# Optimization experiments

Hardware: AMD Instinct MI355X
Metric: run time of the kernel (lower is better)

The kernel has to match this reference:

```python
import jax, jax.numpy as jnp
import numpy as np

B, L, D_MODEL = 2, 2048, 1024
D_STATE, D_CONV, EXPAND = 8, 4, 2
D_INNER = EXPAND * D_MODEL          # 2048
DT_RANK = (D_MODEL + 15) // 16      # 64


def setup_inputs() -> dict:
    key = jax.random.key(0)
    ks = jax.random.split(key, 8)
    s = 0.02
    x = jax.random.normal(ks[0], (B, L, D_MODEL), dtype=jnp.float32)
    W_in = jax.random.normal(ks[1], (D_MODEL, 2 * D_INNER), dtype=jnp.float32) * s
    dw_kernel = jax.random.normal(ks[2], (D_CONV, D_INNER), dtype=jnp.float32) * s  # depthwise
    pw_kernel = jax.random.normal(ks[3], (D_INNER, D_INNER), dtype=jnp.float32) * s  # pointwise
    conv_bias = jnp.zeros((D_INNER,), dtype=jnp.float32)
    W_x = jax.random.normal(ks[4], (D_INNER, DT_RANK + 2 * D_STATE), dtype=jnp.float32) * s
    W_dt = jax.random.normal(ks[5], (DT_RANK, D_INNER), dtype=jnp.float32) * s
    b_dt = jnp.zeros((D_INNER,), dtype=jnp.float32)
    # A = repeat(range(1..d_state), d_inner).reshape(d_inner, d_state), stored as log
    A_init = np.repeat(np.arange(1, D_STATE + 1, dtype=np.float32), D_INNER).reshape(D_INNER, D_STATE)
    A_log = jnp.asarray(np.log(A_init))
    D = jnp.ones((D_INNER,), dtype=jnp.float32)
    W_out = jax.random.normal(ks[6], (D_INNER, D_MODEL), dtype=jnp.float32) * s
    return {"x": x, "W_in": W_in, "dw_kernel": dw_kernel, "pw_kernel": pw_kernel,
            "conv_bias": conv_bias, "W_x": W_x, "W_dt": W_dt, "b_dt": b_dt,
            "A_log": A_log, "D": D, "W_out": W_out}


def reference(x, W_in, dw_kernel, pw_kernel, conv_bias, W_x, W_dt, b_dt, A_log, D, W_out):
    d_inner, d_state = A_log.shape
    dt_rank = W_dt.shape[0]
    d_conv = dw_kernel.shape[0]
    bsz = x.shape[0]

    xz = x @ W_in                                   # [B,L,2*di]
    x_in, z = jnp.split(xz, 2, axis=-1)             # each [B,L,di]

    # causal separable conv: depthwise (causal pad) -> pointwise -> swish
    xp = jnp.pad(x_in, ((0, 0), (d_conv - 1, 0), (0, 0)))
    xc = jax.lax.conv_general_dilated(
        xp, dw_kernel[:, None, :], window_strides=(1,), padding='VALID',
        dimension_numbers=('NWC', 'WIO', 'NWC'), feature_group_count=d_inner)
    xc = jax.nn.silu(xc @ pw_kernel + conv_bias)    # [B,L,di]

    x_dbl = xc @ W_x                                # [B,L,dt_rank+2*ds]
    delta = x_dbl[..., :dt_rank]
    Bm = x_dbl[..., dt_rank:dt_rank + d_state]      # [B,L,ds]
    C = x_dbl[..., dt_rank + d_state:]              # [B,L,ds]
    delta = jax.nn.softplus(delta @ W_dt + b_dt)    # [B,L,di]

    A = -jnp.exp(A_log)                             # [di,ds]
    deltaA = jnp.exp(jnp.einsum('bld,dn->bldn', delta, A))       # [B,L,di,ds]
    deltaB_u = jnp.einsum('bld,bln,bld->bldn', delta, Bm, xc)    # [B,L,di,ds]

    def step(h, inp):
        dA_t, dBu_t, C_t = inp
        h = dA_t * h + dBu_t                        # [B,di,ds]
        y_t = jnp.einsum('bn,bdn->bd', C_t, h)      # [B,di]
        return h, y_t

    h0 = jnp.zeros((bsz, d_inner, d_state), dtype=x.dtype)
    elems = (deltaA.transpose(1, 0, 2, 3), deltaB_u.transpose(1, 0, 2, 3), C.transpose(1, 0, 2))
    _, ys = jax.lax.scan(step, h0, elems)           # ys: [L,B,di]
    y = ys.transpose(1, 0, 2)                       # [B,L,di]

    y = y + xc * D
    y = y * jax.nn.silu(z)
    return y @ W_out                                # [B,L,d_model]
```

## Files before the change

kernel.cpp:

```cpp
#include <hip/hip_runtime.h>
#include <math.h>

#define Bb 2
#define Ll 2048
#define DMODEL 1024
#define DINNER 2048
#define DSTATE 8
#define DTRANK 64
#define DCONV 4
#define MM (Bb*Ll)
#define NCH 64
#define CL 32
#define G3_KCH 8
#define G3_KC (DINNER / G3_KCH)

typedef __attribute__((ext_vector_type(8))) short    bf16x8;
typedef __attribute__((ext_vector_type(4))) float    f32x4;

__device__ __forceinline__ float silu_f(float x) {
    return x / (1.0f + __expf(-x));
}
__device__ __forceinline__ float softplus_f(float x) {
    return fmaxf(x, 0.0f) + log1pf(__expf(-fabsf(x)));
}
__device__ __forceinline__ unsigned short f2bf(float f) {
    unsigned int u = __float_as_uint(f);
    u += 0x7fffu + ((u >> 16) & 1u);
    return (unsigned short)(u >> 16);
}
__device__ __forceinline__ float bf2f(unsigned short u) {
    return __uint_as_float(((unsigned int)u) << 16);
}
__device__ __forceinline__ void async_cp16(const unsigned short* g, unsigned short* l) {
    __builtin_amdgcn_global_load_lds(
        (const __attribute__((address_space(1))) void*)g,
        (__attribute__((address_space(3))) void*)l, 16, 0, 0);
}

template <int EPI, int NW, int TN, typename OT, int RX = 0, int RY = 1>
__global__ __launch_bounds__(NW * 64, 4) void mfma_gemm(
    const unsigned short* __restrict__ A, const unsigned short* __restrict__ Bt,
    OT* __restrict__ C, OT* __restrict__ C2, int nsplit,
    int M, int N, int K, int lda, int ldb, int ldc,
    const float* __restrict__ bias)
{
    constexpr int NT   = NW * 64;
    constexpr int WNC  = NW / 2;
    constexpr int WNE  = TN / WNC;
    constexpr int NJ   = WNE / 16;
    constexpr int RPP  = NT / 4;
    constexpr int APASS = 128 / RPP;
    constexpr int BPASS = TN / RPP;

    __shared__ unsigned short As[2][128 * 32];
    __shared__ unsigned short Bs[2][TN * 32];

    int bxx = blockIdx.x, byy = blockIdx.y;
    if constexpr (RX > 0) {
        const int f = blockIdx.y * gridDim.x + blockIdx.x;
        const int c = f & 7, q = f >> 3;
        const int rgw = gridDim.x / RX;
        bxx = (c % rgw) * RX + (q % RX);
        byy = (c / rgw) * RY + (q / RX);
    }
    const int bm = byy * 128;
    const int bn = bxx * TN;
    const int tid  = threadIdx.x;
    const int w    = tid >> 6;
    const int lane = tid & 63;
    const int wm = (w / WNC) * 64;
    const int wn = (w % WNC) * WNE;
    const int lr = lane & 15;
    const int lq = lane >> 4;

    const int row  = tid >> 2;
    const int sp   = tid & 3;
    const int slog = sp ^ ((row >> 1) & 3);
    const unsigned short* gA = A  + (size_t)(bm + row) * lda + slog * 8;
    const unsigned short* gB = Bt + (size_t)(bn + row) * ldb + slog * 8;
    const int st = tid * 8;

    const int fsw = (lq ^ ((lr >> 1) & 3)) * 8;

    f32x4 acc[4][NJ];
#pragma unroll
    for (int i = 0; i < 4; ++i)
#pragma unroll
        for (int j = 0; j < NJ; ++j) acc[i][j] = (f32x4){0.f, 0.f, 0.f, 0.f};

#pragma unroll
    for (int p = 0; p < APASS; ++p)
        async_cp16(gA + (size_t)p * RPP * lda, &As[0][p * RPP * 32 + st]);
#pragma unroll
    for (int p = 0; p < BPASS; ++p)
        async_cp16(gB + (size_t)p * RPP * ldb, &Bs[0][p * RPP * 32 + st]);

    int cur = 0;
    for (int k0 = 0; k0 < K; k0 += 32, cur ^= 1) {
        __syncthreads();
        const int nk = k0 + 32;
        if (nk < K) {
            const int nb = cur ^ 1;
#pragma unroll
            for (int p = 0; p < APASS; ++p)
                async_cp16(gA + (size_t)p * RPP * lda + nk, &As[nb][p * RPP * 32 + st]);
#pragma unroll
            for (int p = 0; p < BPASS; ++p)
                async_cp16(gB + (size_t)p * RPP * ldb + nk, &Bs[nb][p * RPP * 32 + st]);
        }

        bf16x8 a[4], b[NJ];
#pragma unroll
        for (int i = 0; i < 4; ++i)
            a[i] = *(const bf16x8*)&As[cur][(wm + i * 16 + lr) * 32 + fsw];
#pragma unroll
        for (int j = 0; j < NJ; ++j)
            b[j] = *(const bf16x8*)&Bs[cur][(wn + j * 16 + lr) * 32 + fsw];
#pragma unroll
        for (int i = 0; i < 4; ++i)
#pragma unroll
            for (int j = 0; j < NJ; ++j)
                acc[i][j] = __builtin_amdgcn_mfma_f32_16x16x32_bf16(
                    a[i], b[j], acc[i][j], 0, 0, 0);
    }

#pragma unroll
    for (int i = 0; i < 4; ++i) {
        const int row0 = bm + wm + i * 16 + lq * 4;
#pragma unroll
        for (int j = 0; j < NJ; ++j) {
            const int col = bn + wn + j * 16 + lr;
            OT* Cb; int colb;
            if (col < nsplit) { Cb = C; colb = col; }
            else              { Cb = C2; colb = col - nsplit; }
            float bv = (EPI != 0) ? bias[col] : 0.0f;
#pragma unroll
            for (int r = 0; r < 4; ++r) {
                float v = acc[i][j][r];
                if (EPI == 1) v = silu_f(v + bv);
                if (EPI == 2) v = softplus_f(v + bv);
                if (sizeof(OT) == 2)
                    Cb[(size_t)(row0 + r) * ldc + colb] = (OT)f2bf(v);
                else
                    Cb[(size_t)(row0 + r) * ldc + colb] = (OT)v;
            }
        }
    }
}

template <bool I1, bool I2, int VMA, int VMB>
__device__ __forceinline__ void g1_tile(
    int kt, const unsigned short* __restrict__ gA,
    const unsigned short* __restrict__ gB, int lda, int ldb,
    unsigned short* As, unsigned short* Bs, int st,
    int wm, int wn, int lr, int fsw, f32x4 (&acc)[8][4])
{
    const int cur = kt & 1;
    const int sb0 = (cur << 1) * 8192;
    const int sb1 = ((cur << 1) | 1) * 8192;
    const int nb1 = ((kt + 1) & 1) << 1;
    const int nb2 = ((kt + 2) & 1) << 1;
    bf16x8 a[4], b[4];

#pragma unroll
    for (int i = 0; i < 4; ++i)
        a[i] = *(const bf16x8*)&As[sb0 + (wm + i * 16 + lr) * 32 + fsw];
#pragma unroll
    for (int j = 0; j < 4; ++j)
        b[j] = *(const bf16x8*)&Bs[sb0 + (wn + j * 16 + lr) * 32 + fsw];
    if (I1) {
        const unsigned short* s = gA + (kt + 1) * 64 + 32;
        unsigned short* d = &As[(nb1 | 1) * 8192 + st];
        async_cp16(s, d);
        async_cp16(s + (size_t)128 * lda, d + 4096);
        __builtin_amdgcn_sched_barrier(0);
    }
    __builtin_amdgcn_s_barrier();
    asm volatile("s_waitcnt lgkmcnt(0)" ::: "memory");
    __builtin_amdgcn_sched_barrier(0);
    __builtin_amdgcn_s_setprio(1);
#pragma unroll
    for (int i = 0; i < 4; ++i)
#pragma unroll
        for (int j = 0; j < 4; ++j)
            acc[i][j] = __builtin_amdgcn_mfma_f32_16x16x32_bf16(
                a[i], b[j], acc[i][j], 0, 0, 0);
    __builtin_amdgcn_s_setprio(0);
    __builtin_amdgcn_s_barrier();

#pragma unroll
    for (int i = 0; i < 4; ++i)
        a[i] = *(const bf16x8*)&As[sb0 + (wm + (4 + i) * 16 + lr) * 32 + fsw];
    if (I1) {
        const unsigned short* s = gB + (kt + 1) * 64 + 32;
        unsigned short* d = &Bs[(nb1 | 1) * 8192 + st];
        async_cp16(s, d);
        async_cp16(s + (size_t)128 * ldb, d + 4096);
        __builtin_amdgcn_sched_barrier(0);
    }
    __builtin_amdgcn_s_barrier();
    asm volatile("s_waitcnt lgkmcnt(0)" ::: "memory");
    __builtin_amdgcn_sched_barrier(0);
    __builtin_amdgcn_s_setprio(1);
#pragma unroll
    for (int i = 0; i < 4; ++i)
#pragma unroll
        for (int j = 0; j < 4; ++j)
            acc[4 + i][j] = __builtin_amdgcn_mfma_f32_16x16x32_bf16(
                a[i], b[j], acc[4 + i][j], 0, 0, 0);
    __builtin_amdgcn_s_setprio(0);
    asm volatile("s_waitcnt vmcnt(%0)" :: "n"(VMA) : "memory");
    __builtin_amdgcn_s_barrier();

#pragma unroll
    for (int i = 0; i < 4; ++i)
        a[i] = *(const bf16x8*)&As[sb1 + (wm + i * 16 + lr) * 32 + fsw];
#pragma unroll
    for (int j = 0; j < 4; ++j)
        b[j] = *(const bf16x8*)&Bs[sb1 + (wn + j * 16 + lr) * 32 + fsw];
    if (I2) {
        const unsigned short* s = gA + (kt + 2) * 64;
        unsigned short* d = &As[nb2 * 8192 + st];
        async_cp16(s, d);
        async_cp16(s + (size_t)128 * lda, d + 4096);
        __builtin_amdgcn_sched_barrier(0);
    }
    __builtin_amdgcn_s_barrier();
    asm volatile("s_waitcnt lgkmcnt(0)" ::: "memory");
    __builtin_amdgcn_sched_barrier(0);
    __builtin_amdgcn_s_setprio(1);
#pragma unroll
    for (int i = 0; i < 4; ++i)
#pragma unroll
        for (int j = 0; j < 4; ++j)
            acc[i][j] = __builtin_amdgcn_mfma_f32_16x16x32_bf16(
                a[i], b[j], acc[i][j], 0, 0, 0);
    __builtin_amdgcn_s_setprio(0);
    __builtin_amdgcn_s_barrier();

#pragma unroll
    for (int i = 0; i < 4; ++i)
        a[i] = *(const bf16x8*)&As[sb1 + (wm + (4 + i) * 16 + lr) * 32 + fsw];
    if (I2) {
        const unsigned short* s = gB + (kt + 2) * 64;
        unsigned short* d = &Bs[nb2 * 8192 + st];
        async_cp16(s, d);
        async_cp16(s + (size_t)128 * ldb, d + 4096);
        __builtin_amdgcn_sched_barrier(0);
    }
    __builtin_amdgcn_s_barrier();
    asm volatile("s_waitcnt lgkmcnt(0)" ::: "memory");
    __builtin_amdgcn_sched_barrier(0);
    __builtin_amdgcn_s_setprio(1);
#pragma unroll
    for (int i = 0; i < 4; ++i)
#pragma unroll
        for (int j = 0; j < 4; ++j)
            acc[4 + i][j] = __builtin_amdgcn_mfma_f32_16x16x32_bf16(
                a[i], b[j], acc[4 + i][j], 0, 0, 0);
    __builtin_amdgcn_s_setprio(0);
    asm volatile("s_waitcnt vmcnt(%0)" :: "n"(VMB) : "memory");
    __builtin_amdgcn_s_barrier();
}

__global__ __launch_bounds__(512, 2) void gemm256_g1(
    const unsigned short* __restrict__ A, const unsigned short* __restrict__ Bt,
    unsigned short* __restrict__ Cx, unsigned short* __restrict__ Cz,
    int K, int lda, int ldb, int ldc, int nsplit)
{
    __shared__ unsigned short As[4 * 8192];
    __shared__ unsigned short Bs[4 * 8192];

    int bx, by;
    {
        const int f = blockIdx.y * gridDim.x + blockIdx.x;
        const int c = f & 7, q = f >> 3;
        const int rgw = gridDim.x >> 3;
        bx = (c % rgw) * 8 + (q & 7);
        by = (c / rgw) * 4 + (q >> 3);
    }
    const int bm = by * 256, bn = bx * 256;
    const int tid  = threadIdx.x;
    const int lane = tid & 63;
    const int w    = tid >> 6;
    const int wm = (w >> 2) << 7;
    const int wn = (w & 3) << 6;
    const int lr = lane & 15;
    const int lq = lane >> 4;
    const int fsw = (lq ^ ((lr >> 1) & 3)) * 8;

    const int row  = tid >> 2;
    const int slog = (tid & 3) ^ ((row >> 1) & 3);
    const unsigned short* gA = A  + (size_t)(bm + row) * lda + slog * 8;
    const unsigned short* gB = Bt + (size_t)(bn + row) * ldb + slog * 8;
    const int st = tid * 8;
    const int NT = K >> 6;

    f32x4 acc[8][4];
#pragma unroll
    for (int i = 0; i < 8; ++i)
#pragma unroll
        for (int j = 0; j < 4; ++j) acc[i][j] = (f32x4){0.f, 0.f, 0.f, 0.f};

    auto stg = [&](const unsigned short* g, int ld, unsigned short* d) {
        async_cp16(g, d);
        async_cp16(g + (size_t)128 * ld, d + 4096);
    };
    stg(gA,      lda, As + 0 * 8192 + st);
    __builtin_amdgcn_sched_barrier(0);
    stg(gB,      ldb, Bs + 0 * 8192 + st);
    __builtin_amdgcn_sched_barrier(0);
    stg(gA + 32, lda, As + 1 * 8192 + st);
    __builtin_amdgcn_sched_barrier(0);
    stg(gB + 32, ldb, Bs + 1 * 8192 + st);
    __builtin_amdgcn_sched_barrier(0);
    stg(gA + 64, lda, As + 2 * 8192 + st);
    __builtin_amdgcn_sched_barrier(0);
    stg(gB + 64, ldb, Bs + 2 * 8192 + st);
    asm volatile("s_waitcnt vmcnt(8)" ::: "memory");
    __builtin_amdgcn_sched_barrier(0);
    __builtin_amdgcn_s_barrier();

    for (int kt = 0; kt + 2 < NT; ++kt)
        g1_tile<true, true, 8, 8>(kt, gA, gB, lda, ldb,
                                  As, Bs, st, wm, wn, lr, fsw, acc);
    g1_tile<true,  false, 8, 4>(NT - 2, gA, gB, lda, ldb,
                                As, Bs, st, wm, wn, lr, fsw, acc);
    g1_tile<false, false, 0, 0>(NT - 1, gA, gB, lda, ldb,
                                As, Bs, st, wm, wn, lr, fsw, acc);

#pragma unroll
    for (int i = 0; i < 8; ++i) {
        const int row0 = bm + wm + i * 16 + lq * 4;
#pragma unroll
        for (int j = 0; j < 4; ++j) {
            const int col = bn + wn + j * 16 + lr;
            unsigned short* Cb; int colb;
            if (col < nsplit) { Cb = Cx; colb = col; }
            else              { Cb = Cz; colb = col - nsplit; }
#pragma unroll
            for (int r = 0; r < 4; ++r)
                Cb[(size_t)(row0 + r) * ldc + colb] = f2bf(acc[i][j][r]);
        }
    }
}

template <bool I1, bool I2, int VMA, int VMB>
__device__ __forceinline__ void g2c_tile(
    int kt, const unsigned short* __restrict__ gA,
    const unsigned short* __restrict__ gB, int lda, int ldb,
    unsigned short* As, unsigned short* Bs, int st,
    int wm, int wn, int lr, int fsw, f32x4 (&acc)[4][4])
{
    const int cur = kt & 1;
    const int sa0 = (cur << 1) * 4096;
    const int sa1 = ((cur << 1) | 1) * 4096;
    const int sb0 = (cur << 1) * 4096;
    const int sb1 = ((cur << 1) | 1) * 4096;
    const int nb1 = (((kt + 1) & 1) << 1) | 1;
    const int nb2 = ((kt + 2) & 1) << 1;
    bf16x8 a[4], b[4];

#pragma unroll
    for (int i = 0; i < 4; ++i)
        a[i] = *(const bf16x8*)&As[sa0 + (wm + i * 16 + lr) * 32 + fsw];
#pragma unroll
    for (int j = 0; j < 4; ++j)
        b[j] = *(const bf16x8*)&Bs[sb0 + (wn + j * 16 + lr) * 32 + fsw];
    if (I1) {
        const unsigned short* sA = gA + (kt + 1) * 64 + 32;
        unsigned short* dA = &As[nb1 * 4096 + st];
        async_cp16(sA, dA);
        async_cp16(sA + (size_t)64 * lda, dA + 2048);
        const unsigned short* sB = gB + (kt + 1) * 64 + 32;
        unsigned short* dB = &Bs[nb1 * 4096 + st];
        async_cp16(sB, dB);
        async_cp16(sB + (size_t)64 * ldb, dB + 2048);
        __builtin_amdgcn_sched_barrier(0);
    }
    __builtin_amdgcn_s_barrier();
    asm volatile("s_waitcnt lgkmcnt(0)" ::: "memory");
    __builtin_amdgcn_sched_barrier(0);
    __builtin_amdgcn_s_setprio(1);
#pragma unroll
    for (int i = 0; i < 4; ++i)
#pragma unroll
        for (int j = 0; j < 4; ++j)
            acc[i][j] = __builtin_amdgcn_mfma_f32_16x16x32_bf16(
                a[i], b[j], acc[i][j], 0, 0, 0);
    __builtin_amdgcn_s_setprio(0);
    asm volatile("s_waitcnt vmcnt(%0)" :: "n"(VMA) : "memory");
    __builtin_amdgcn_s_barrier();

#pragma unroll
    for (int i = 0; i < 4; ++i)
        a[i] = *(const bf16x8*)&As[sa1 + (wm + i * 16 + lr) * 32 + fsw];
#pragma unroll
    for (int j = 0; j < 4; ++j)
        b[j] = *(const bf16x8*)&Bs[sb1 + (wn + j * 16 + lr) * 32 + fsw];
    if (I2) {
        const unsigned short* sA = gA + (kt + 2) * 64;
        unsigned short* dA = &As[nb2 * 4096 + st];
        async_cp16(sA, dA);
        async_cp16(sA + (size_t)64 * lda, dA + 2048);
        const unsigned short* sB = gB + (kt + 2) * 64;
        unsigned short* dB = &Bs[nb2 * 4096 + st];
        async_cp16(sB, dB);
        async_cp16(sB + (size_t)64 * ldb, dB + 2048);
        __builtin_amdgcn_sched_barrier(0);
    }
    __builtin_amdgcn_s_barrier();
    asm volatile("s_waitcnt lgkmcnt(0)" ::: "memory");
    __builtin_amdgcn_sched_barrier(0);
    __builtin_amdgcn_s_setprio(1);
#pragma unroll
    for (int i = 0; i < 4; ++i)
#pragma unroll
        for (int j = 0; j < 4; ++j)
            acc[i][j] = __builtin_amdgcn_mfma_f32_16x16x32_bf16(
                a[i], b[j], acc[i][j], 0, 0, 0);
    __builtin_amdgcn_s_setprio(0);
    asm volatile("s_waitcnt vmcnt(%0)" :: "n"(VMB) : "memory");
    __builtin_amdgcn_s_barrier();
}

template <int EPI, typename OT>
__global__ __launch_bounds__(256, 2) void gemm128x128(
    const unsigned short* __restrict__ A, const unsigned short* __restrict__ Bt,
    OT* __restrict__ C, int K, int lda, int ldb, int ldc,
    const float* __restrict__ bias)
{
    __shared__ unsigned short As[4 * 4096];
    __shared__ unsigned short Bs[4 * 4096];

    int bx, by;
    {
        const int f = blockIdx.y * gridDim.x + blockIdx.x;
        const int c = f & 7, q = f >> 3;
        const int rgw = gridDim.x >> 3;
        bx = (c % rgw) * 8 + (q & 7);
        by = (c / rgw) * 8 + (q >> 3);
    }
    const int bm = by * 128, bn = bx * 128;
    const int tid  = threadIdx.x;
    const int lane = tid & 63;
    const int w    = tid >> 6;
    const int wm = (w >> 1) << 6;
    const int wn = (w & 1) << 6;
    const int lr = lane & 15;
    const int lq = lane >> 4;
    const int fsw = (lq ^ ((lr >> 1) & 3)) * 8;

    const int row  = tid >> 2;
    const int slog = (tid & 3) ^ ((row >> 1) & 3);
    const unsigned short* gA = A  + (size_t)(bm + row) * lda + slog * 8;
    const unsigned short* gB = Bt + (size_t)(bn + row) * ldb + slog * 8;
    const int st = tid * 8;
    const int NT = K >> 6;

    f32x4 acc[4][4];
#pragma unroll
    for (int i = 0; i < 4; ++i)
#pragma unroll
        for (int j = 0; j < 4; ++j) acc[i][j] = (f32x4){0.f, 0.f, 0.f, 0.f};

    auto stg = [&](int ko, int slot) {
        const unsigned short* sA = gA + ko;
        unsigned short* dA = &As[slot * 4096 + st];
        async_cp16(sA, dA);
        async_cp16(sA + (size_t)64 * lda, dA + 2048);
        const unsigned short* sB = gB + ko;
        unsigned short* dB = &Bs[slot * 4096 + st];
        async_cp16(sB, dB);
        async_cp16(sB + (size_t)64 * ldb, dB + 2048);
    };
    stg(0, 0);
    __builtin_amdgcn_sched_barrier(0);
    stg(32, 1);
    __builtin_amdgcn_sched_barrier(0);
    stg(64, 2);
    asm volatile("s_waitcnt vmcnt(8)" ::: "memory");
    __builtin_amdgcn_sched_barrier(0);
    __builtin_amdgcn_s_barrier();

    for (int kt = 0; kt + 2 < NT; ++kt)
        g2c_tile<true, true, 8, 8>(kt, gA, gB, lda, ldb,
                                   As, Bs, st, wm, wn, lr, fsw, acc);
    g2c_tile<true,  false, 8, 4>(NT - 2, gA, gB, lda, ldb,
                                 As, Bs, st, wm, wn, lr, fsw, acc);
    g2c_tile<false, false, 0, 0>(NT - 1, gA, gB, lda, ldb,
                                 As, Bs, st, wm, wn, lr, fsw, acc);

#pragma unroll
    for (int i = 0; i < 4; ++i) {
        const int row0 = bm + wm + i * 16 + lq * 4;
#pragma unroll
        for (int j = 0; j < 4; ++j) {
            const int col = bn + wn + j * 16 + lr;
            float bv = (EPI != 0) ? bias[col] : 0.0f;
#pragma unroll
            for (int r = 0; r < 4; ++r) {
                float v = acc[i][j][r];
                if (EPI == 1) v = silu_f(v + bv);
                if (EPI == 2) v = softplus_f(v + bv);
                if (sizeof(OT) == 2)
                    C[(size_t)(row0 + r) * ldc + col] = (OT)f2bf(v);
                else
                    C[(size_t)(row0 + r) * ldc + col] = (OT)v;
            }
        }
    }
}

__global__ __launch_bounds__(256) void prep_all(
    const float* __restrict__ x, const float* __restrict__ W_in,
    const float* __restrict__ pwk, const float* __restrict__ W_out,
    const float* __restrict__ W_dt,
    unsigned short* __restrict__ x_bf, unsigned short* __restrict__ Wint,
    unsigned short* __restrict__ pw_t, unsigned short* __restrict__ Woutt,
    unsigned short* __restrict__ Wdtt)
{
    const int b = blockIdx.x;
    const int t = threadIdx.x;
    if (b < 4096) {
        int i = b * 1024 + t * 4;
        float4 v = *(const float4*)&x[i];
        ushort4 o;
        o.x = f2bf(v.x); o.y = f2bf(v.y); o.z = f2bf(v.z); o.w = f2bf(v.w);
        *(ushort4*)&x_bf[i] = o;
        return;
    }
    const float* src; unsigned short* dst; int R, C, c0, r0;
    if (b < 8192) {
        int bi = b - 4096; src = W_in; dst = Wint; R = 1024; C = 4096;
        c0 = (bi & 127) * 32; r0 = (bi >> 7) * 32;
    } else if (b < 12288) {
        int bi = b - 8192; src = pwk; dst = pw_t; R = 2048; C = 2048;
        c0 = (bi & 63) * 32; r0 = (bi >> 6) * 32;
    } else if (b < 14336) {
        int bi = b - 12288; src = W_out; dst = Woutt; R = 2048; C = 1024;
        c0 = (bi & 31) * 32; r0 = (bi >> 5) * 32;
    } else {
        int bi = b - 14336; src = W_dt; dst = Wdtt; R = 64; C = 2048;
        c0 = (bi & 63) * 32; r0 = (bi >> 6) * 32;
    }
    __shared__ float tile[32][33];
    const int tx = t & 31;
    const int ty = t >> 5;
#pragma unroll
    for (int i = 0; i < 32; i += 8)
        tile[ty + i][tx] = src[(size_t)(r0 + ty + i) * C + c0 + tx];
    __syncthreads();
#pragma unroll
    for (int i = 0; i < 32; i += 8)
        dst[(size_t)(c0 + ty + i) * R + r0 + tx] = f2bf(tile[tx][ty + i]);
}

__global__ __launch_bounds__(256) void g3_splitk(
    const unsigned short* __restrict__ xc, const float* __restrict__ Wx,
    float* __restrict__ part)
{
    __shared__ float As[16][68];
    __shared__ float Bs[16][85];
    const int m0 = blockIdx.x * 64;
    const int kb = blockIdx.y * G3_KC;
    const int t = threadIdx.x;
    const int tr = t >> 4;
    const int tc = t & 15;

    const int arow = t >> 2;
    const int ak4  = (t & 3) * 4;
    const int bk   = t >> 4;
    const int bc   = (t & 15) * 5;

    float acc[4][5];
#pragma unroll
    for (int r = 0; r < 4; ++r)
#pragma unroll
        for (int c = 0; c < 5; ++c) acc[r][c] = 0.0f;

    for (int k0 = 0; k0 < G3_KC; k0 += 16) {
        ushort4 av = *(const ushort4*)&xc[(size_t)(m0 + arow) * DINNER + kb + k0 + ak4];
        float bv[5];
#pragma unroll
        for (int q = 0; q < 5; ++q)
            bv[q] = Wx[(size_t)(kb + k0 + bk) * 80 + bc + q];
        __syncthreads();
        As[ak4 + 0][arow] = bf2f(av.x);
        As[ak4 + 1][arow] = bf2f(av.y);
        As[ak4 + 2][arow] = bf2f(av.z);
        As[ak4 + 3][arow] = bf2f(av.w);
#pragma unroll
        for (int q = 0; q < 5; ++q) Bs[bk][bc + q] = bv[q];
        __syncthreads();
#pragma unroll
        for (int k = 0; k < 16; ++k) {
            float a[4], b[5];
#pragma unroll
            for (int r = 0; r < 4; ++r) a[r] = As[k][tr * 4 + r];
#pragma unroll
            for (int c = 0; c < 5; ++c) b[c] = Bs[k][tc * 5 + c];
#pragma unroll
            for (int r = 0; r < 4; ++r)
#pragma unroll
                for (int c = 0; c < 5; ++c)
                    acc[r][c] = fmaf(a[r], b[c], acc[r][c]);
        }
    }
#pragma unroll
    for (int r = 0; r < 4; ++r)
#pragma unroll
        for (int c = 0; c < 5; ++c)
            part[((size_t)blockIdx.y * MM + m0 + tr * 4 + r) * 80 + tc * 5 + c] = acc[r][c];
}

__global__ __launch_bounds__(256) void g3_reduce(
    const float* __restrict__ part, float* __restrict__ xdbl,
    unsigned short* __restrict__ xdbl64)
{
    int i = (blockIdx.x * 256 + threadIdx.x) * 4;
    if (i >= MM * 80) return;
    float4 s = *(const float4*)&part[i];
#pragma unroll
    for (int c = 1; c < G3_KCH; ++c) {
        float4 p = *(const float4*)&part[(size_t)c * MM * 80 + i];
        s.x += p.x; s.y += p.y; s.z += p.z; s.w += p.w;
    }
    *(float4*)&xdbl[i] = s;
    int col = i % 80;
    if (col < 64) {
        int row = i / 80;
        ushort4 o;
        o.x = f2bf(s.x); o.y = f2bf(s.y); o.z = f2bf(s.z); o.w = f2bf(s.w);
        *(ushort4*)&xdbl64[(size_t)row * 64 + col] = o;
    }
}

__global__ __launch_bounds__(256) void dwconv_kernel(
    const unsigned short* __restrict__ x_in, const float* __restrict__ dwk,
    unsigned short* __restrict__ out)
{
    int i4 = blockIdx.x * 256 + threadIdx.x;
    if (i4 >= MM * DINNER / 4) return;
    int d = (i4 * 4) & (DINNER - 1);
    int bl = (i4 * 4) >> 11;
    int l = bl & (Ll - 1);
    int b = bl >> 11;
    float a0 = 0.f, a1 = 0.f, a2 = 0.f, a3 = 0.f;
#pragma unroll
    for (int k = 0; k < DCONV; ++k) {
        int t = l + k - (DCONV - 1);
        if (t >= 0) {
            ushort4 xv = *(const ushort4*)&x_in[(size_t)(b * Ll + t) * DINNER + d];
            float4 wv = *(const float4*)&dwk[k * DINNER + d];
            a0 = fmaf(bf2f(xv.x), wv.x, a0);
            a1 = fmaf(bf2f(xv.y), wv.y, a1);
            a2 = fmaf(bf2f(xv.z), wv.z, a2);
            a3 = fmaf(bf2f(xv.w), wv.w, a3);
        }
    }
    ushort4 o;
    o.x = f2bf(a0); o.y = f2bf(a1); o.z = f2bf(a2); o.w = f2bf(a3);
    *(ushort4*)&out[i4 * 4] = o;
}

__global__ __launch_bounds__(256) void scan_pass1(
    const float* __restrict__ delta, const unsigned short* __restrict__ xc,
    const float* __restrict__ xdbl, const float* __restrict__ A_log,
    float* __restrict__ cs_a, float* __restrict__ cs_h)
{
    const int d = blockIdx.x * 256 + threadIdx.x;
    const int c = blockIdx.y;
    const int b = blockIdx.z;
    const int t0 = c * CL;

    __shared__ float sB[CL][8];
    {
        int i = threadIdx.x;
        int t = i >> 3, j = i & 7;
        sB[t][j] = xdbl[((size_t)(b * Ll + t0 + t)) * 80 + DTRANK + j];
    }
    __syncthreads();

    float An[8];
#pragma unroll
    for (int n = 0; n < 8; ++n) An[n] = -__expf(A_log[d * 8 + n]);

    float h[8], ap[8];
#pragma unroll
    for (int n = 0; n < 8; ++n) { h[n] = 0.0f; ap[n] = 1.0f; }

    const float* dptr = delta + ((size_t)(b * Ll + t0)) * DINNER + d;
    const unsigned short* xptr = xc + ((size_t)(b * Ll + t0)) * DINNER + d;

#pragma unroll 4
    for (int t = 0; t < CL; ++t) {
        float dl = dptr[(size_t)t * DINNER];
        float xv = bf2f(xptr[(size_t)t * DINNER]);
        float du = dl * xv;
#pragma unroll
        for (int n = 0; n < 8; ++n) {
            float dA = __expf(dl * An[n]);
            h[n] = fmaf(dA, h[n], du * sB[t][n]);
            ap[n] *= dA;
        }
    }

    size_t base = (((size_t)(b * NCH + c)) * 8) * DINNER + d;
#pragma unroll
    for (int n = 0; n < 8; ++n) {
        cs_a[base + (size_t)n * DINNER] = ap[n];
        cs_h[base + (size_t)n * DINNER] = h[n];
    }
}

__global__ __launch_bounds__(256) void scan_pass2(
    const float* __restrict__ cs_a, const float* cs_h, float* hin)
{
    int idx = blockIdx.x * 256 + threadIdx.x;
    if (idx >= Bb * 8 * DINNER) return;
    int d = idx & (DINNER - 1);
    int n = (idx >> 11) & 7;
    int b = idx >> 14;
    float H = 0.0f;
#pragma unroll 4
    for (int c = 0; c < NCH; ++c) {
        size_t o = (((size_t)(b * NCH + c)) * 8 + n) * DINNER + d;
        float a = cs_a[o];
        float hh = cs_h[o];
        hin[o] = H;
        H = fmaf(a, H, hh);
    }
}

__global__ __launch_bounds__(256) void scan_pass3(
    const float* __restrict__ delta, const unsigned short* __restrict__ xc,
    const float* __restrict__ xdbl, const float* __restrict__ A_log,
    const float* __restrict__ hin, const unsigned short* __restrict__ z,
    const float* __restrict__ Dvec, unsigned short* __restrict__ y_bf)
{
    const int d = blockIdx.x * 256 + threadIdx.x;
    const int c = blockIdx.y;
    const int b = blockIdx.z;
    const int t0 = c * CL;

    __shared__ float sB[CL][8];
    __shared__ float sC[CL][8];
    {
        int i = threadIdx.x;
        int t = i >> 4, j = i & 15;
        float v = xdbl[((size_t)(b * Ll + t0 + t)) * 80 + DTRANK + j];
        if (j < 8) sB[t][j] = v; else sC[t][j - 8] = v;
        t = (i + 256) >> 4; j = (i + 256) & 15;
        v = xdbl[((size_t)(b * Ll + t0 + t)) * 80 + DTRANK + j];
        if (j < 8) sB[t][j] = v; else sC[t][j - 8] = v;
    }
    __syncthreads();

    float An[8];
#pragma unroll
    for (int n = 0; n < 8; ++n) An[n] = -__expf(A_log[d * 8 + n]);

    float h[8];
    size_t hbase = (((size_t)(b * NCH + c)) * 8) * DINNER + d;
#pragma unroll
    for (int n = 0; n < 8; ++n) h[n] = hin[hbase + (size_t)n * DINNER];

    const float Dd = Dvec[d];
    const float* dptr = delta + ((size_t)(b * Ll + t0)) * DINNER + d;
    const unsigned short* xptr = xc + ((size_t)(b * Ll + t0)) * DINNER + d;
    const unsigned short* zptr = z + ((size_t)(b * Ll + t0)) * DINNER + d;
    unsigned short* yptr = y_bf + ((size_t)(b * Ll + t0)) * DINNER + d;

    for (int t = 0; t < CL; ++t) {
        float dl = dptr[(size_t)t * DINNER];
        float xv = bf2f(xptr[(size_t)t * DINNER]);
        float du = dl * xv;
        float yt = 0.0f;
#pragma unroll
        for (int n = 0; n < 8; ++n) {
            float dA = __expf(dl * An[n]);
            h[n] = fmaf(dA, h[n], du * sB[t][n]);
            yt = fmaf(sC[t][n], h[n], yt);
        }
        float zv = bf2f(zptr[(size_t)t * DINNER]);
        yptr[(size_t)t * DINNER] = f2bf((yt + xv * Dd) * silu_f(zv));
    }
}

extern "C" void kernel_launch(void* const* d_in, const int* in_sizes, int n_in,
                              void* d_out, int out_size, void* d_ws, size_t ws_size,
                              hipStream_t stream)
{
    const float* x         = (const float*)d_in[0];
    const float* W_in      = (const float*)d_in[1];
    const float* dwk       = (const float*)d_in[2];
    const float* pwk       = (const float*)d_in[3];
    const float* conv_bias = (const float*)d_in[4];
    const float* W_x       = (const float*)d_in[5];
    const float* W_dt      = (const float*)d_in[6];
    const float* b_dt      = (const float*)d_in[7];
    const float* A_log     = (const float*)d_in[8];
    const float* Dv        = (const float*)d_in[9];
    const float* W_out     = (const float*)d_in[10];
    float* out = (float*)d_out;

    char* ws = (char*)d_ws;
    unsigned short* x_in_bf = (unsigned short*)(ws);
    unsigned short* z_bf    = (unsigned short*)(ws + (16ull << 20));
    float*          delta   = (float*)(ws + (32ull << 20));
    unsigned short* x_bf    = (unsigned short*)(ws + (64ull << 20));
    unsigned short* y_bf    = (unsigned short*)(ws + (64ull << 20));
    unsigned short* Wint    = (unsigned short*)(ws + (72ull << 20));
    unsigned short* pw_t    = (unsigned short*)(ws + (80ull << 20));
    unsigned short* xcp_bf  = (unsigned short*)(ws + (88ull << 20));
    unsigned short* xc_bf   = (unsigned short*)(ws + (104ull << 20));
    unsigned short* Woutt   = (unsigned short*)(ws + (120ull << 20));
    float*          xdbl    = (float*)(ws + (124ull << 20));
    unsigned short* xdbl64  = (unsigned short*)(ws + (125ull << 20) + (512ull << 10));
    float*          g3part  = (float*)(ws + (126ull << 20));
    float*          cs_a    = (float*)(ws + (136ull << 20));
    float*          cs_h    = (float*)(ws + (144ull << 20));
    unsigned short* Wdtt    = (unsigned short*)(ws + (152ull << 20));
    float*          hin     = cs_h;
    dim3 blk(256);

    prep_all<<<14464, blk, 0, stream>>>(x, W_in, pwk, W_out, W_dt,
                                        x_bf, Wint, pw_t, Woutt, Wdtt);

    gemm256_g1<<<dim3((2 * DINNER) / 256, MM / 256), dim3(512), 0, stream>>>(
        x_bf, Wint, x_in_bf, z_bf,
        DMODEL, DMODEL, DMODEL, DINNER,
        DINNER);

    dwconv_kernel<<<MM * DINNER / 4 / 256, blk, 0, stream>>>(x_in_bf, dwk, xcp_bf);

    gemm128x128<1, unsigned short>
        <<<dim3(DINNER / 128, MM / 128), blk, 0, stream>>>(
        xcp_bf, pw_t, xc_bf,
        DINNER, DINNER, DINNER, DINNER, conv_bias);

    g3_splitk<<<dim3(MM / 64, G3_KCH), blk, 0, stream>>>(xc_bf, W_x, g3part);
    g3_reduce<<<(MM * 80 / 4 + 255) / 256, blk, 0, stream>>>(g3part, xdbl, xdbl64);

    mfma_gemm<2, 4, 64, float>
        <<<dim3(DINNER / 64, MM / 128), blk, 0, stream>>>(
        xdbl64, Wdtt, delta, delta, DINNER + 1,
        MM, DINNER, DTRANK, DTRANK, DTRANK, DINNER, b_dt);

    scan_pass1<<<dim3(DINNER / 256, NCH, Bb), blk, 0, stream>>>(
        delta, xc_bf, xdbl, A_log, cs_a, cs_h);
    scan_pass2<<<(Bb * 8 * DINNER + 255) / 256, blk, 0, stream>>>(cs_a, cs_h, hin);
    scan_pass3<<<dim3(DINNER / 256, NCH, Bb), blk, 0, stream>>>(
        delta, xc_bf, xdbl, A_log, hin, z_bf, Dv, y_bf);

    mfma_gemm<0, 4, 64, float, 8, 8>
        <<<dim3(DMODEL / 64, MM / 128), blk, 0, stream>>>(
        y_bf, Woutt, out, out, DMODEL + 1,
        MM, DMODEL, DINNER, DINNER, DINNER, DMODEL, nullptr);
}
```

Baseline: 359.6 us.

## Store delta in bf16 and vectorize weight transpose-convert loads/stores

The delta buffer produced by the dt-projection GEMM is now written as bf16 instead of fp32, and both scan passes read and widen it, halving delta traffic in the scan. Separately, the prep transpose kernel now loads float4 rows and writes ushort4 packed bf16 outputs with a single pass per thread instead of four strided scalar iterations. The bf16 delta loses precision in the softplus output feeding exp in the scan, which may affect accuracy.

```diff
diff --git a/kernel.cpp b/kernel.cpp
--- a/kernel.cpp
+++ b/kernel.cpp
@@ -545,15 +545,26 @@
         c0 = (bi & 63) * 32; r0 = (bi >> 6) * 32;
     }
     __shared__ float tile[32][33];
-    const int tx = t & 31;
-    const int ty = t >> 5;
-#pragma unroll
-    for (int i = 0; i < 32; i += 8)
-        tile[ty + i][tx] = src[(size_t)(r0 + ty + i) * C + c0 + tx];
+    {
+        const int rx = (t & 7) * 4;
+        const int ry = t >> 3;
+        float4 v = *(const float4*)&src[(size_t)(r0 + ry) * C + c0 + rx];
+        tile[ry][rx + 0] = v.x;
+        tile[ry][rx + 1] = v.y;
+        tile[ry][rx + 2] = v.z;
+        tile[ry][rx + 3] = v.w;
+    }
     __syncthreads();
-#pragma unroll
-    for (int i = 0; i < 32; i += 8)
-        dst[(size_t)(c0 + ty + i) * R + r0 + tx] = f2bf(tile[tx][ty + i]);
+    {
+        const int wx = (t & 7) * 4;
+        const int wy = t >> 3;
+        ushort4 o;
+        o.x = f2bf(tile[wx + 0][wy]);
+        o.y = f2bf(tile[wx + 1][wy]);
+        o.z = f2bf(tile[wx + 2][wy]);
+        o.w = f2bf(tile[wx + 3][wy]);
+        *(ushort4*)&dst[(size_t)(c0 + wy) * R + r0 + wx] = o;
+    }
 }
 
 __global__ __launch_bounds__(256) void g3_splitk(
@@ -665,7 +676,7 @@
 }
 
 __global__ __launch_bounds__(256) void scan_pass1(
-    const float* __restrict__ delta, const unsigned short* __restrict__ xc,
+    const unsigned short* __restrict__ delta, const unsigned short* __restrict__ xc,
     const float* __restrict__ xdbl, const float* __restrict__ A_log,
     float* __restrict__ cs_a, float* __restrict__ cs_h)
 {
@@ -690,12 +701,12 @@
 #pragma unroll
     for (int n = 0; n < 8; ++n) { h[n] = 0.0f; ap[n] = 1.0f; }
 
-    const float* dptr = delta + ((size_t)(b * Ll + t0)) * DINNER + d;
+    const unsigned short* dptr = delta + ((size_t)(b * Ll + t0)) * DINNER + d;
     const unsigned short* xptr = xc + ((size_t)(b * Ll + t0)) * DINNER + d;
 
 #pragma unroll 4
     for (int t = 0; t < CL; ++t) {
-        float dl = dptr[(size_t)t * DINNER];
+        float dl = bf2f(dptr[(size_t)t * DINNER]);
         float xv = bf2f(xptr[(size_t)t * DINNER]);
         float du = dl * xv;
 #pragma unroll
@@ -734,7 +745,7 @@
 }
 
 __global__ __launch_bounds__(256) void scan_pass3(
-    const float* __restrict__ delta, const unsigned short* __restrict__ xc,
+    const unsigned short* __restrict__ delta, const unsigned short* __restrict__ xc,
     const float* __restrict__ xdbl, const float* __restrict__ A_log,
     const float* __restrict__ hin, const unsigned short* __restrict__ z,
     const float* __restrict__ Dvec, unsigned short* __restrict__ y_bf)
@@ -767,13 +778,13 @@
     for (int n = 0; n < 8; ++n) h[n] = hin[hbase + (size_t)n * DINNER];
 
     const float Dd = Dvec[d];
-    const float* dptr = delta + ((size_t)(b * Ll + t0)) * DINNER + d;
+    const unsigned short* dptr = delta + ((size_t)(b * Ll + t0)) * DINNER + d;
     const unsigned short* xptr = xc + ((size_t)(b * Ll + t0)) * DINNER + d;
     const unsigned short* zptr = z + ((size_t)(b * Ll + t0)) * DINNER + d;
     unsigned short* yptr = y_bf + ((size_t)(b * Ll + t0)) * DINNER + d;
 
     for (int t = 0; t < CL; ++t) {
-        float dl = dptr[(size_t)t * DINNER];
+        float dl = bf2f(dptr[(size_t)t * DINNER]);
         float xv = bf2f(xptr[(size_t)t * DINNER]);
         float du = dl * xv;
         float yt = 0.0f;
@@ -808,7 +819,7 @@
     char* ws = (char*)d_ws;
     unsigned short* x_in_bf = (unsigned short*)(ws);
     unsigned short* z_bf    = (unsigned short*)(ws + (16ull << 20));
-    float*          delta   = (float*)(ws + (32ull << 20));
+    unsigned short* delta   = (unsigned short*)(ws + (32ull << 20));
     unsigned short* x_bf    = (unsigned short*)(ws + (64ull << 20));
     unsigned short* y_bf    = (unsigned short*)(ws + (64ull << 20));
     unsigned short* Wint    = (unsigned short*)(ws + (72ull << 20));
@@ -843,7 +854,7 @@
     g3_splitk<<<dim3(MM / 64, G3_KCH), blk, 0, stream>>>(xc_bf, W_x, g3part);
     g3_reduce<<<(MM * 80 / 4 + 255) / 256, blk, 0, stream>>>(g3part, xdbl, xdbl64);
 
-    mfma_gemm<2, 4, 64, float>
+    mfma_gemm<2, 4, 64, unsigned short>
         <<<dim3(DINNER / 64, MM / 128), blk, 0, stream>>>(
         xdbl64, Wdtt, delta, delta, DINNER + 1,
         MM, DINNER, DTRANK, DTRANK, DTRANK, DINNER, b_dt);
```

Measured after the change: 362.5 us. No clear change (+0.8%).
